# Kernel optimization log

Measured on AMD Instinct MI355X. Metric: run time of the kernel, lower is better.

## Reference

```python
import jax, jax.numpy as jnp
import numpy as np

B, N, C = 128, 1024, 1
N_TIMES = 2
NUM_SUBSTEPS = 279  # trunc(dt_Output/dt_sub)+1 for default params


def setup_inputs() -> dict:
    key = jax.random.key(0)
    # small amplitude: d_to_u multiplies spectrum by k (up to N/2), keep CFL stable
    x = jax.random.normal(key, (B, N, C), dtype=jnp.float32) * 1e-3
    return {
        "x": x,
        "nu_para": jnp.float32(-3.0),
        "dt_Output_para": jnp.float32(-3.0),
        "cRatio_para": jnp.float32(0.1),
        "nTimes": N_TIMES,
        "num_substeps": NUM_SUBSTEPS,
    }


def _forward(x, nu_para, dt_Output_para, cRatio_para, nTimes, num_substeps):
    n = x.shape[1]
    L = 2.0 * np.pi
    k = (2.0 * np.pi / L) * jnp.arange(n // 2 + 1, dtype=jnp.float32)  # [n//2+1]
    ik = 1j * k

    # reparameterized physical params (sigmoid squashing, as in the torch module)
    nu = jax.nn.sigmoid(nu_para) * (0.5 - 0.01) + 0.01
    dt_out = jax.nn.sigmoid(dt_Output_para) * (0.1 - 0.001) + 0.001
    cR = jax.nn.sigmoid(cRatio_para) * (2.0 - 0.5) + 0.5

    d = jnp.transpose(x, (0, 2, 1))  # [B, C, N]
    # d_to_u: u = irfft(1j * rfft(d) * k)
    u = jnp.fft.irfft(1j * jnp.fft.rfft(d) * k, n=n)

    dt = dt_out / num_substeps
    # q = 1 - dt*cR*(k + nu*(1j*k)^2) ; (1j*k)^2 = -k^2 so q is real-valued
    q = 1.0 - dt * cR * (k - nu * k * k)

    def substep(u, _):
        uhat = jnp.fft.rfft(u)
        u2hat = jnp.fft.rfft(0.5 * u * u)
        u_new = jnp.fft.irfft((uhat - dt * ik * u2hat) / q, n=n)
        return u_new, None

    def outer(u, _):
        u, _ = jax.lax.scan(substep, u, None, length=num_substeps)
        return u, u

    _, usol = jax.lax.scan(outer, u, None, length=nTimes)  # [T, B, C, N]
    T = usol.shape[0]
    # torch.cat(usol, dim=1): [B, T*C, N] with time-major ordering
    usol = jnp.moveaxis(usol, 0, 1).reshape(usol.shape[1], T * usol.shape[2], n)

    # u_to_d: d_hat = -1j*rfft(u); d_hat[...,1:] /= k[1:]; d_hat[...,0] = 0
    d_hat = -1j * jnp.fft.rfft(usol)
    safe_k = jnp.where(k > 0, k, 1.0)
    d_hat = jnp.where(k > 0, d_hat / safe_k, jnp.zeros((), dtype=d_hat.dtype))
    dsol = jnp.fft.irfft(d_hat, n=n)  # [B, T*C, N]

    return jnp.transpose(dsol, (0, 2, 1))  # [B, N, T*C]


def reference(x, nu_para, dt_Output_para, cRatio_para, nTimes, num_substeps):
    return _forward(x, nu_para, dt_Output_para, cRatio_para, nTimes, num_substeps)
```

## Files before the change

### kernel.cpp

```cpp
#include <hip/hip_runtime.h>
#include <math.h>

#define NFFT 1024
#define BLK  512

template <int CTRL>
__device__ __forceinline__ float dppf(float v) {
    return __int_as_float(__builtin_amdgcn_update_dpp(
        0, __float_as_int(v), CTRL, 0xF, 0xF, true));
}
__device__ __forceinline__ float qx1(float v) { return dppf<0xB1>(v); }
__device__ __forceinline__ float qx2(float v) { return dppf<0x4E>(v); }
__device__ __forceinline__ float xr4(float v) { return dppf<0x1B>(dppf<0x141>(v)); }
__device__ __forceinline__ float xr8(float v) { return dppf<0x128>(v); }

__device__ __forceinline__ void pswap16(float v, float& lo, float& hi) {
    auto r = __builtin_amdgcn_permlane16_swap(__float_as_int(v), __float_as_int(v),
                                              false, false);
    lo = __int_as_float(r[0]);
    hi = __int_as_float(r[1]);
}
__device__ __forceinline__ void pswap32(float v, float& lo, float& hi) {
    auto r = __builtin_amdgcn_permlane32_swap(__float_as_int(v), __float_as_int(v),
                                              false, false);
    lo = __int_as_float(r[0]);
    hi = __int_as_float(r[1]);
}

__global__ __launch_bounds__(BLK, 2)
void siva_kernel(const float* __restrict__ x,
                 const float* __restrict__ nu_p,
                 const float* __restrict__ dto_p,
                 const float* __restrict__ cr_p,
                 const int* __restrict__ nt_p,
                 const int* __restrict__ ns_p,
                 float* __restrict__ out) {
    __shared__ float4 bufF[BLK];
    __shared__ float4 bufI[BLK];

    const int tt = threadIdx.x;
    const int b  = blockIdx.x;
    const int l  = tt & 63;
    const int w  = tt >> 6;
    const int R  = (int)(__brev((unsigned)l) >> 26);

    const int nT   = nt_p[0];
    const int nsub = ns_p[0];

    const float nu  = (1.0f / (1.0f + expf(-nu_p[0])))  * (0.5f - 0.01f)  + 0.01f;
    const float dto = (1.0f / (1.0f + expf(-dto_p[0]))) * (0.1f - 0.001f) + 0.001f;
    const float cR  = (1.0f / (1.0f + expf(-cr_p[0])))  * (2.0f - 0.5f)   + 0.5f;
    const float dt   = dto / (float)nsub;
    const float dtcR = dt * cR;

    float2 T10;
    { const float a = (float)tt * (1.0f / 512.0f);
      T10 = make_float2(cospif(a), -sinpif(a)); }

    float2 E8f[8], D8[8];
    #pragma unroll
    for (int j = 0; j < 8; ++j) {
        const float af = (float)(j * w) * 0.25f + (float)(l * w) * (1.0f / 256.0f);
        E8f[j] = make_float2(cospif(af), -sinpif(af));
        const float ai = (float)(w * j) * 0.25f + (float)(l * j) * (1.0f / 256.0f);
        D8[j] = make_float2(cospif(ai), sinpif(ai));
    }

    float2 wf[6]; float sg[6]; float2 wi[6];
    #pragma unroll
    for (int s = 0; s < 6; ++s) {
        const int h = 32 >> s;
        const int lm = l & (h - 1);
        const bool hif = (l & h) != 0;
        const float a = (float)(lm * (32 / h)) * (1.0f / 32.0f);
        wf[s] = hif ? make_float2(cospif(a), -sinpif(a)) : make_float2(1.0f, 0.0f);
        sg[s] = hif ? -1.0f : 1.0f;
        const int h2 = 1 << s;
        const int lm2 = l & (h2 - 1);
        const float a2 = (float)lm2 / (float)h2;
        float2 wb = make_float2(cospif(a2), sinpif(a2));
        if ((l & h2) != 0) { wb.x = -wb.x; wb.y = -wb.y; }
        wi[s] = wb;
    }
    const bool m2 = (l & 2) != 0, m4 = (l & 4) != 0, m8 = (l & 8) != 0;

    float Sc[2], csn[2], si[2];
    #pragma unroll
    for (int p = 0; p < 2; ++p) {
        const int k = 16 * R + 2 * w + p;
        const float kk = (k <= 512) ? (float)k : (float)(k - 1024);
        const float ka = fabsf(kk);
        const float q  = 1.0f - dtcR * (ka - nu * ka * ka);
        const float a  = (1.0f / q) * (1.0f / 1024.0f);
        const float kkS = (k == 0 || k == 512) ? 0.0f : kk;
        Sc[p]  = a * (1.0f - dt * kkS);
        csn[p] = (k == 0) ? 0.0f : (1.0f / (1024.0f * kk));
        si[p]  = kk * (1.0f / 1024.0f);
    }
    float A2[2], B2[2];
    { const float sg1 = (l & 1) ? -1.0f : 1.0f;
      #pragma unroll
      for (int p = 0; p < 2; ++p) {
          const float so = __shfl_xor(Sc[p], 1);
          A2[p] = Sc[p] + so;
          B2[p] = sg1 * (Sc[p] - so);
      } }

    auto fwd_s = [&](float2& zz, float bx, float by, int s) {
        const float tx = fmaf(sg[s], zz.x, bx);
        const float ty = fmaf(sg[s], zz.y, by);
        zz.x = tx * wf[s].x - ty * wf[s].y;
        zz.y = tx * wf[s].y + ty * wf[s].x;
    };
    auto inv_s = [&](float2& zz, float bx, float by, int s, bool hi) {
        const float px = hi ? zz.x : bx, py = hi ? zz.y : by;
        const float qx = hi ? bx : zz.x, qy = hi ? by : zz.y;
        zz.x = qx + px * wi[s].x - py * wi[s].y;
        zz.y = qy + px * wi[s].y + py * wi[s].x;
    };

    auto lane_fwd5 = [&](float2 z[2]) {
        #pragma unroll
        for (int r = 0; r < 2; ++r) {
            float lox, hix, loy, hiy;
            pswap32(z[r].x, lox, hix); pswap32(z[r].y, loy, hiy);
            const float tx = fmaf(sg[0], hix, lox);
            const float ty = fmaf(sg[0], hiy, loy);
            z[r].x = tx * wf[0].x - ty * wf[0].y;
            z[r].y = tx * wf[0].y + ty * wf[0].x;
        }
        #pragma unroll
        for (int r = 0; r < 2; ++r) {
            float lox, hix, loy, hiy;
            pswap16(z[r].x, lox, hix); pswap16(z[r].y, loy, hiy);
            const float tx = fmaf(sg[1], hix, lox);
            const float ty = fmaf(sg[1], hiy, loy);
            z[r].x = tx * wf[1].x - ty * wf[1].y;
            z[r].y = tx * wf[1].y + ty * wf[1].x;
        }
        #pragma unroll
        for (int r = 0; r < 2; ++r) fwd_s(z[r], xr8(z[r].x), xr8(z[r].y), 2);
        #pragma unroll
        for (int r = 0; r < 2; ++r) fwd_s(z[r], xr4(z[r].x), xr4(z[r].y), 3);
        #pragma unroll
        for (int r = 0; r < 2; ++r) fwd_s(z[r], qx2(z[r].x), qx2(z[r].y), 4);
    };
    auto lane_inv5 = [&](float2 z[2]) {
        #pragma unroll
        for (int r = 0; r < 2; ++r) inv_s(z[r], qx2(z[r].x), qx2(z[r].y), 1, m2);
        #pragma unroll
        for (int r = 0; r < 2; ++r) inv_s(z[r], xr4(z[r].x), xr4(z[r].y), 2, m4);
        #pragma unroll
        for (int r = 0; r < 2; ++r) inv_s(z[r], xr8(z[r].x), xr8(z[r].y), 3, m8);
        #pragma unroll
        for (int r = 0; r < 2; ++r) {
            float lox, hix, loy, hiy;
            pswap16(z[r].x, lox, hix); pswap16(z[r].y, loy, hiy);
            z[r].x = fmaf(wi[4].x, hix, fmaf(-wi[4].y, hiy, lox));
            z[r].y = fmaf(wi[4].x, hiy, fmaf( wi[4].y, hix, loy));
        }
        #pragma unroll
        for (int r = 0; r < 2; ++r) {
            float lox, hix, loy, hiy;
            pswap32(z[r].x, lox, hix); pswap32(z[r].y, loy, hiy);
            z[r].x = fmaf(wi[5].x, hix, fmaf(-wi[5].y, hiy, lox));
            z[r].y = fmaf(wi[5].x, hiy, fmaf( wi[5].y, hix, loy));
        }
    };

    auto fwd_head = [&](float2 z[2]) {
        const float2 A  = make_float2(z[0].x + z[1].x, z[0].y + z[1].y);
        const float2 Dm = make_float2(z[0].x - z[1].x, z[0].y - z[1].y);
        const float2 Bc = make_float2(Dm.x * T10.x - Dm.y * T10.y,
                                      Dm.x * T10.y + Dm.y * T10.x);
        bufF[tt] = make_float4(A.x, A.y, Bc.x, Bc.y);
        __syncthreads();
        float2 za = make_float2(0.0f, 0.0f), zb = make_float2(0.0f, 0.0f);
        #pragma unroll
        for (int j = 0; j < 8; ++j) {
            const float4 v = bufF[64 * j + l];
            za.x = fmaf(E8f[j].x, v.x, za.x);  za.x = fmaf(-E8f[j].y, v.y, za.x);
            za.y = fmaf(E8f[j].x, v.y, za.y);  za.y = fmaf(E8f[j].y, v.x, za.y);
            zb.x = fmaf(E8f[j].x, v.z, zb.x);  zb.x = fmaf(-E8f[j].y, v.w, zb.x);
            zb.y = fmaf(E8f[j].x, v.w, zb.y);  zb.y = fmaf(E8f[j].y, v.z, zb.y);
        }
        z[0] = za; z[1] = zb;
        lane_fwd5(z);
    };

    auto inv_tail = [&](float2 z[2], float& u0o, float& u1o) {
        lane_inv5(z);
        bufI[tt] = make_float4(z[0].x, z[0].y, z[1].x, z[1].y);
        __syncthreads();
        float vAx = 0.0f, vBx = 0.0f, vBy = 0.0f;
        #pragma unroll
        for (int j = 0; j < 8; ++j) {
            const float4 v = bufI[64 * j + l];
            vAx = fmaf(D8[j].x, v.x, vAx);  vAx = fmaf(-D8[j].y, v.y, vAx);
            vBx = fmaf(D8[j].x, v.z, vBx);  vBx = fmaf(-D8[j].y, v.w, vBx);
            vBy = fmaf(D8[j].x, v.w, vBy);  vBy = fmaf(D8[j].y, v.z, vBy);
        }
        const float re = vBx * T10.x + vBy * T10.y;
        u0o = vAx + re;
        u1o = vAx - re;
    };

    float2 z[2];
    float u0, u1;
    z[0] = make_float2(x[b * NFFT + tt], 0.0f);
    z[1] = make_float2(x[b * NFFT + tt + 512], 0.0f);
    fwd_head(z);
    #pragma unroll
    for (int r = 0; r < 2; ++r) fwd_s(z[r], qx1(z[r].x), qx1(z[r].y), 5);
    #pragma unroll
    for (int p = 0; p < 2; ++p) {
        const float zx = z[p].x, zy = z[p].y;
        z[p] = make_float2(-zy * si[p], zx * si[p]);
    }
    { const bool m1 = (l & 1) != 0;
      #pragma unroll
      for (int r = 0; r < 2; ++r) inv_s(z[r], qx1(z[r].x), qx1(z[r].y), 0, m1); }
    inv_tail(z, u0, u1);

    for (int ot = 0; ot < nT; ++ot) {
        for (int ss = 0; ss < nsub; ++ss) {
            z[0] = make_float2(u0, 0.5f * u0 * u0);
            z[1] = make_float2(u1, 0.5f * u1 * u1);
            fwd_head(z);
            #pragma unroll
            for (int p = 0; p < 2; ++p) {
                const float px = qx1(z[p].x), py = qx1(z[p].y);
                z[p].x = fmaf(A2[p], z[p].x, B2[p] * px);
                z[p].y = fmaf(A2[p], z[p].y, B2[p] * py);
            }
            inv_tail(z, u0, u1);
        }
        z[0] = make_float2(u0, 0.0f);
        z[1] = make_float2(u1, 0.0f);
        fwd_head(z);
        #pragma unroll
        for (int r = 0; r < 2; ++r) fwd_s(z[r], qx1(z[r].x), qx1(z[r].y), 5);
        #pragma unroll
        for (int p = 0; p < 2; ++p) {
            const float zx = z[p].x, zy = z[p].y;
            z[p] = make_float2(zy * csn[p], -zx * csn[p]);
        }
        { const bool m1 = (l & 1) != 0;
          #pragma unroll
          for (int r = 0; r < 2; ++r) inv_s(z[r], qx1(z[r].x), qx1(z[r].y), 0, m1); }
        float d0, d1;
        inv_tail(z, d0, d1);
        out[(b * NFFT + tt) * nT + ot]       = d0;
        out[(b * NFFT + tt + 512) * nT + ot] = d1;
    }
}

extern "C" void kernel_launch(void* const* d_in, const int* in_sizes, int n_in,
                              void* d_out, int out_size, void* d_ws, size_t ws_size,
                              hipStream_t stream) {
    const float* x     = (const float*)d_in[0];
    const float* nu_p  = (const float*)d_in[1];
    const float* dto_p = (const float*)d_in[2];
    const float* cr_p  = (const float*)d_in[3];
    const int*   nt_p  = (const int*)d_in[4];
    const int*   ns_p  = (const int*)d_in[5];
    float* out = (float*)d_out;

    const int B = in_sizes[0] / NFFT;
    siva_kernel<<<B, BLK, 0, stream>>>(x, nu_p, dto_p, cr_p, nt_p, ns_p, out);
}
```

Baseline: 701.9 us.

## Fold last two FFT stages and spectral multiply into precomputed 4-lane matrix

Replaces the per-substep forward radix-2 stage 4, the diagonal spectral update, and inverse stages 0-1 with a single precomputed complex 4x4 quad-lane mixing matrix applied via DPP swizzles. It also rewrites the 8-point DFT in the forward head as a radix-2 factorized butterfly instead of a direct 8-term sum, and merges the per-stage twiddle select in inverse stages 2-3 into precomputed coefficient pairs. This cuts DPP and FMA work on the serial per-substep path. In exchange it adds register pressure from the precomputed matrices and a different floating-point rounding order.

New measurement: 707.3 us. Within noise of the previous version (+0.8%).

```diff
diff --git a/kernel.cpp b/kernel.cpp
--- a/kernel.cpp
+++ b/kernel.cpp
@@ -11,6 +11,7 @@
 }
 __device__ __forceinline__ float qx1(float v) { return dppf<0xB1>(v); }
 __device__ __forceinline__ float qx2(float v) { return dppf<0x4E>(v); }
+__device__ __forceinline__ float qx3(float v) { return dppf<0x1B>(v); }
 __device__ __forceinline__ float xr4(float v) { return dppf<0x1B>(dppf<0x141>(v)); }
 __device__ __forceinline__ float xr8(float v) { return dppf<0x128>(v); }
 
@@ -57,11 +58,18 @@
     { const float a = (float)tt * (1.0f / 512.0f);
       T10 = make_float2(cospif(a), -sinpif(a)); }
 
-    float2 E8f[8], D8[8];
+    const float pm = (w & 1) ? -1.0f : 1.0f;
+    float2 c4w, w8w, rotf;
+    { const float aw = 0.5f * (float)w;
+      c4w = make_float2(cospif(aw), -sinpif(aw));
+      const float aw8 = 0.25f * (float)w;
+      w8w = make_float2(cospif(aw8), -sinpif(aw8));
+      const float ar = (float)(l * w) * (1.0f / 256.0f);
+      rotf = make_float2(cospif(ar), -sinpif(ar)); }
+
+    float2 D8[8];
     #pragma unroll
     for (int j = 0; j < 8; ++j) {
-        const float af = (float)(j * w) * 0.25f + (float)(l * w) * (1.0f / 256.0f);
-        E8f[j] = make_float2(cospif(af), -sinpif(af));
         const float ai = (float)(w * j) * 0.25f + (float)(l * j) * (1.0f / 256.0f);
         D8[j] = make_float2(cospif(ai), sinpif(ai));
     }
@@ -82,7 +90,16 @@
         if ((l & h2) != 0) { wb.x = -wb.x; wb.y = -wb.y; }
         wi[s] = wb;
     }
-    const bool m2 = (l & 2) != 0, m4 = (l & 4) != 0, m8 = (l & 8) != 0;
+    const bool m1 = (l & 1) != 0, m2 = (l & 2) != 0,
+               m4 = (l & 4) != 0, m8 = (l & 8) != 0;
+
+    float2 cai[2], cbi[2];
+    #pragma unroll
+    for (int s = 2; s <= 3; ++s) {
+        const bool hif = (l & (1 << s)) != 0;
+        cai[s - 2] = hif ? wi[s] : make_float2(1.0f, 0.0f);
+        cbi[s - 2] = hif ? make_float2(1.0f, 0.0f) : wi[s];
+    }
 
     float Sc[2], csn[2], si[2];
     #pragma unroll
@@ -97,14 +114,41 @@
         csn[p] = (k == 0) ? 0.0f : (1.0f / (1024.0f * kk));
         si[p]  = kk * (1.0f / 1024.0f);
     }
-    float A2[2], B2[2];
-    { const float sg1 = (l & 1) ? -1.0f : 1.0f;
-      #pragma unroll
-      for (int p = 0; p < 2; ++p) {
-          const float so = __shfl_xor(Sc[p], 1);
-          A2[p] = Sc[p] + so;
-          B2[p] = sg1 * (Sc[p] - so);
-      } }
+
+    float2 Cq[2][4];
+    {
+        auto compose = [&](float2* o, const float2* bb, const float2* aa) {
+            #pragma unroll
+            for (int e = 0; e < 4; ++e) {
+                float cx = 0.0f, cy = 0.0f;
+                #pragma unroll
+                for (int d = 0; d < 4; ++d) {
+                    const float ax = __shfl_xor(aa[d ^ e].x, d);
+                    const float ay = __shfl_xor(aa[d ^ e].y, d);
+                    cx = fmaf(bb[d].x, ax, fmaf(-bb[d].y, ay, cx));
+                    cy = fmaf(bb[d].x, ay, fmaf(bb[d].y, ax, cy));
+                }
+                o[e] = make_float2(cx, cy);
+            }
+        };
+        const float2 one = make_float2(1.0f, 0.0f);
+        const float2 zer = make_float2(0.0f, 0.0f);
+        float2 Arow[4] = { make_float2(wf[4].x * sg[4], wf[4].y * sg[4]), zer,
+                           wf[4], zer };
+        float2 Brow[4] = { make_float2(sg[5], 0.0f), one, zer, zer };
+        float2 Erow[4] = { m1 ? wi[0] : one, m1 ? one : wi[0], zer, zer };
+        float2 Frow[4] = { m2 ? wi[1] : one, zer, m2 ? one : wi[1], zer };
+        float2 M1[4], M2[4], M3[4];
+        compose(M1, Brow, Arow);
+        #pragma unroll
+        for (int p = 0; p < 2; ++p) {
+            #pragma unroll
+            for (int e = 0; e < 4; ++e)
+                M2[e] = make_float2(Sc[p] * M1[e].x, Sc[p] * M1[e].y);
+            compose(M3, Erow, M2);
+            compose(Cq[p], Frow, M3);
+        }
+    }
 
     auto fwd_s = [&](float2& zz, float bx, float by, int s) {
         const float tx = fmaf(sg[s], zz.x, bx);
@@ -119,7 +163,7 @@
         zz.y = qy + px * wi[s].y + py * wi[s].x;
     };
 
-    auto lane_fwd5 = [&](float2 z[2]) {
+    auto lane_fwd4 = [&](float2 z[2]) {
         #pragma unroll
         for (int r = 0; r < 2; ++r) {
             float lox, hix, loy, hiy;
@@ -142,16 +186,26 @@
         for (int r = 0; r < 2; ++r) fwd_s(z[r], xr8(z[r].x), xr8(z[r].y), 2);
         #pragma unroll
         for (int r = 0; r < 2; ++r) fwd_s(z[r], xr4(z[r].x), xr4(z[r].y), 3);
-        #pragma unroll
-        for (int r = 0; r < 2; ++r) fwd_s(z[r], qx2(z[r].x), qx2(z[r].y), 4);
-    };
-    auto lane_inv5 = [&](float2 z[2]) {
-        #pragma unroll
-        for (int r = 0; r < 2; ++r) inv_s(z[r], qx2(z[r].x), qx2(z[r].y), 1, m2);
-        #pragma unroll
-        for (int r = 0; r < 2; ++r) inv_s(z[r], xr4(z[r].x), xr4(z[r].y), 2, m4);
-        #pragma unroll
-        for (int r = 0; r < 2; ++r) inv_s(z[r], xr8(z[r].x), xr8(z[r].y), 3, m8);
+    };
+    auto lane_inv4 = [&](float2 z[2]) {
+        #pragma unroll
+        for (int r = 0; r < 2; ++r) {
+            const float px = xr4(z[r].x), py = xr4(z[r].y);
+            const float nx = fmaf(cai[0].x, z[r].x, fmaf(-cai[0].y, z[r].y,
+                             fmaf(cbi[0].x, px, -cbi[0].y * py)));
+            const float ny = fmaf(cai[0].x, z[r].y, fmaf(cai[0].y, z[r].x,
+                             fmaf(cbi[0].x, py, cbi[0].y * px)));
+            z[r] = make_float2(nx, ny);
+        }
+        #pragma unroll
+        for (int r = 0; r < 2; ++r) {
+            const float px = xr8(z[r].x), py = xr8(z[r].y);
+            const float nx = fmaf(cai[1].x, z[r].x, fmaf(-cai[1].y, z[r].y,
+                             fmaf(cbi[1].x, px, -cbi[1].y * py)));
+            const float ny = fmaf(cai[1].x, z[r].y, fmaf(cai[1].y, z[r].x,
+                             fmaf(cbi[1].x, py, cbi[1].y * px)));
+            z[r] = make_float2(nx, ny);
+        }
         #pragma unroll
         for (int r = 0; r < 2; ++r) {
             float lox, hix, loy, hiy;
@@ -165,6 +219,24 @@
             pswap32(z[r].x, lox, hix); pswap32(z[r].y, loy, hiy);
             z[r].x = fmaf(wi[5].x, hix, fmaf(-wi[5].y, hiy, lox));
             z[r].y = fmaf(wi[5].x, hiy, fmaf( wi[5].y, hix, loy));
+        }
+    };
+
+    auto stageQuadC = [&](float2 z[2]) {
+        #pragma unroll
+        for (int p = 0; p < 2; ++p) {
+            const float x1 = qx1(z[p].x), y1 = qx1(z[p].y);
+            const float x2 = qx2(z[p].x), y2 = qx2(z[p].y);
+            const float x3 = qx3(z[p].x), y3 = qx3(z[p].y);
+            float nx = Cq[p][0].x * z[p].x - Cq[p][0].y * z[p].y;
+            float ny = Cq[p][0].x * z[p].y + Cq[p][0].y * z[p].x;
+            nx = fmaf(Cq[p][1].x, x1, fmaf(-Cq[p][1].y, y1, nx));
+            ny = fmaf(Cq[p][1].x, y1, fmaf( Cq[p][1].y, x1, ny));
+            nx = fmaf(Cq[p][2].x, x2, fmaf(-Cq[p][2].y, y2, nx));
+            ny = fmaf(Cq[p][2].x, y2, fmaf( Cq[p][2].y, x2, ny));
+            nx = fmaf(Cq[p][3].x, x3, fmaf(-Cq[p][3].y, y3, nx));
+            ny = fmaf(Cq[p][3].x, y3, fmaf( Cq[p][3].y, x3, ny));
+            z[p] = make_float2(nx, ny);
         }
     };
 
@@ -175,26 +247,49 @@
                                       Dm.x * T10.y + Dm.y * T10.x);
         bufF[tt] = make_float4(A.x, A.y, Bc.x, Bc.y);
         __syncthreads();
-        float2 za = make_float2(0.0f, 0.0f), zb = make_float2(0.0f, 0.0f);
-        #pragma unroll
-        for (int j = 0; j < 8; ++j) {
-            const float4 v = bufF[64 * j + l];
-            za.x = fmaf(E8f[j].x, v.x, za.x);  za.x = fmaf(-E8f[j].y, v.y, za.x);
-            za.y = fmaf(E8f[j].x, v.y, za.y);  za.y = fmaf(E8f[j].y, v.x, za.y);
-            zb.x = fmaf(E8f[j].x, v.z, zb.x);  zb.x = fmaf(-E8f[j].y, v.w, zb.x);
-            zb.y = fmaf(E8f[j].x, v.w, zb.y);  zb.y = fmaf(E8f[j].y, v.z, zb.y);
-        }
-        z[0] = za; z[1] = zb;
-        lane_fwd5(z);
+        float4 v[8];
+        #pragma unroll
+        for (int j = 0; j < 8; ++j) v[j] = bufF[64 * j + l];
+        {
+            const float a0x = fmaf(pm, v[4].x, v[0].x), a0y = fmaf(pm, v[4].y, v[0].y);
+            const float a1x = fmaf(pm, v[6].x, v[2].x), a1y = fmaf(pm, v[6].y, v[2].y);
+            const float a2x = fmaf(pm, v[5].x, v[1].x), a2y = fmaf(pm, v[5].y, v[1].y);
+            const float a3x = fmaf(pm, v[7].x, v[3].x), a3y = fmaf(pm, v[7].y, v[3].y);
+            const float Ex = fmaf(c4w.x, a1x, fmaf(-c4w.y, a1y, a0x));
+            const float Ey = fmaf(c4w.x, a1y, fmaf( c4w.y, a1x, a0y));
+            const float Fx = fmaf(c4w.x, a3x, fmaf(-c4w.y, a3y, a2x));
+            const float Fy = fmaf(c4w.x, a3y, fmaf( c4w.y, a3x, a2y));
+            const float Sx = fmaf(w8w.x, Fx, fmaf(-w8w.y, Fy, Ex));
+            const float Sy = fmaf(w8w.x, Fy, fmaf( w8w.y, Fx, Ey));
+            z[0] = make_float2(Sx * rotf.x - Sy * rotf.y,
+                               Sx * rotf.y + Sy * rotf.x);
+        }
+        {
+            const float a0x = fmaf(pm, v[4].z, v[0].z), a0y = fmaf(pm, v[4].w, v[0].w);
+            const float a1x = fmaf(pm, v[6].z, v[2].z), a1y = fmaf(pm, v[6].w, v[2].w);
+            const float a2x = fmaf(pm, v[5].z, v[1].z), a2y = fmaf(pm, v[5].w, v[1].w);
+            const float a3x = fmaf(pm, v[7].z, v[3].z), a3y = fmaf(pm, v[7].w, v[3].w);
+            const float Ex = fmaf(c4w.x, a1x, fmaf(-c4w.y, a1y, a0x));
+            const float Ey = fmaf(c4w.x, a1y, fmaf( c4w.y, a1x, a0y));
+            const float Fx = fmaf(c4w.x, a3x, fmaf(-c4w.y, a3y, a2x));
+            const float Fy = fmaf(c4w.x, a3y, fmaf( c4w.y, a3x, a2y));
+            const float Sx = fmaf(w8w.x, Fx, fmaf(-w8w.y, Fy, Ex));
+            const float Sy = fmaf(w8w.x, Fy, fmaf( w8w.y, Fx, Ey));
+            z[1] = make_float2(Sx * rotf.x - Sy * rotf.y,
+                               Sx * rotf.y + Sy * rotf.x);
+        }
+        lane_fwd4(z);
     };
 
     auto inv_tail = [&](float2 z[2], float& u0o, float& u1o) {
-        lane_inv5(z);
+        lane_inv4(z);
         bufI[tt] = make_float4(z[0].x, z[0].y, z[1].x, z[1].y);
         __syncthreads();
-        float vAx = 0.0f, vBx = 0.0f, vBy = 0.0f;
-        #pragma unroll
-        for (int j = 0; j < 8; ++j) {
+        float vAx, vBx, vBy;
+        { const float4 v0 = bufI[l];
+          vAx = v0.x; vBx = v0.z; vBy = v0.w; }
+        #pragma unroll
+        for (int j = 1; j < 8; ++j) {
             const float4 v = bufI[64 * j + l];
             vAx = fmaf(D8[j].x, v.x, vAx);  vAx = fmaf(-D8[j].y, v.y, vAx);
             vBx = fmaf(D8[j].x, v.z, vBx);  vBx = fmaf(-D8[j].y, v.w, vBx);
@@ -211,15 +306,18 @@
     z[1] = make_float2(x[b * NFFT + tt + 512], 0.0f);
     fwd_head(z);
     #pragma unroll
+    for (int r = 0; r < 2; ++r) fwd_s(z[r], qx2(z[r].x), qx2(z[r].y), 4);
+    #pragma unroll
     for (int r = 0; r < 2; ++r) fwd_s(z[r], qx1(z[r].x), qx1(z[r].y), 5);
     #pragma unroll
     for (int p = 0; p < 2; ++p) {
         const float zx = z[p].x, zy = z[p].y;
         z[p] = make_float2(-zy * si[p], zx * si[p]);
     }
-    { const bool m1 = (l & 1) != 0;
-      #pragma unroll
-      for (int r = 0; r < 2; ++r) inv_s(z[r], qx1(z[r].x), qx1(z[r].y), 0, m1); }
+    #pragma unroll
+    for (int r = 0; r < 2; ++r) inv_s(z[r], qx1(z[r].x), qx1(z[r].y), 0, m1);
+    #pragma unroll
+    for (int r = 0; r < 2; ++r) inv_s(z[r], qx2(z[r].x), qx2(z[r].y), 1, m2);
     inv_tail(z, u0, u1);
 
     for (int ot = 0; ot < nT; ++ot) {
@@ -227,27 +325,25 @@
             z[0] = make_float2(u0, 0.5f * u0 * u0);
             z[1] = make_float2(u1, 0.5f * u1 * u1);
             fwd_head(z);
-            #pragma unroll
-            for (int p = 0; p < 2; ++p) {
-                const float px = qx1(z[p].x), py = qx1(z[p].y);
-                z[p].x = fmaf(A2[p], z[p].x, B2[p] * px);
-                z[p].y = fmaf(A2[p], z[p].y, B2[p] * py);
-            }
+            stageQuadC(z);
             inv_tail(z, u0, u1);
         }
         z[0] = make_float2(u0, 0.0f);
         z[1] = make_float2(u1, 0.0f);
         fwd_head(z);
         #pragma unroll
+        for (int r = 0; r < 2; ++r) fwd_s(z[r], qx2(z[r].x), qx2(z[r].y), 4);
+        #pragma unroll
         for (int r = 0; r < 2; ++r) fwd_s(z[r], qx1(z[r].x), qx1(z[r].y), 5);
         #pragma unroll
         for (int p = 0; p < 2; ++p) {
             const float zx = z[p].x, zy = z[p].y;
             z[p] = make_float2(zy * csn[p], -zx * csn[p]);
         }
-        { const bool m1 = (l & 1) != 0;
-          #pragma unroll
-          for (int r = 0; r < 2; ++r) inv_s(z[r], qx1(z[r].x), qx1(z[r].y), 0, m1); }
+        #pragma unroll
+        for (int r = 0; r < 2; ++r) inv_s(z[r], qx1(z[r].x), qx1(z[r].y), 0, m1);
+        #pragma unroll
+        for (int r = 0; r < 2; ++r) inv_s(z[r], qx2(z[r].x), qx2(z[r].y), 1, m2);
         float d0, d1;
         inv_tail(z, d0, d1);
         out[(b * NFFT + tt) * nT + ot]       = d0;
```

## Fuse spectral multiply into single LDS exchange via precomputed circulant rows

Applied to the files above, without the earlier changes.

Each substep now does a 64-point in-lane FFT, then one LDS exchange, then a 64-point inverse. Before, it did two exchanges with separate 8-point DFT stages plus a spectral multiply. The diagonal spectral operator and the 8-point outer stages are folded into per-thread 16x2 complex coefficient rows, built once with trig at setup. This halves the __syncthreads and LDS round trips per substep and drops the twiddle/T10 work. In exchange it adds more FMAs per exchange (a 16-point dense mix instead of 8), more registers for the 64 floats of coefficients, and costly one-time row construction that could hurt occupancy.

Result: slower. 2.652 ms (+277.9%).

```diff
diff --git a/kernel.cpp b/kernel.cpp
--- a/kernel.cpp
+++ b/kernel.cpp
@@ -35,14 +35,15 @@
                  const int* __restrict__ nt_p,
                  const int* __restrict__ ns_p,
                  float* __restrict__ out) {
-    __shared__ float4 bufF[BLK];
-    __shared__ float4 bufI[BLK];
+    __shared__ float4 buf[2][BLK];
 
     const int tt = threadIdx.x;
     const int b  = blockIdx.x;
     const int l  = tt & 63;
     const int w  = tt >> 6;
-    const int R  = (int)(__brev((unsigned)l) >> 26);
+    const int a0 = 2 * w;
+    const int a1 = 2 * w + 1;
+    const int kb = (int)(__brev((unsigned)l) >> 26);
 
     const int nT   = nt_p[0];
     const int nsub = ns_p[0];
@@ -52,19 +53,6 @@
     const float cR  = (1.0f / (1.0f + expf(-cr_p[0])))  * (2.0f - 0.5f)   + 0.5f;
     const float dt   = dto / (float)nsub;
     const float dtcR = dt * cR;
-
-    float2 T10;
-    { const float a = (float)tt * (1.0f / 512.0f);
-      T10 = make_float2(cospif(a), -sinpif(a)); }
-
-    float2 E8f[8], D8[8];
-    #pragma unroll
-    for (int j = 0; j < 8; ++j) {
-        const float af = (float)(j * w) * 0.25f + (float)(l * w) * (1.0f / 256.0f);
-        E8f[j] = make_float2(cospif(af), -sinpif(af));
-        const float ai = (float)(w * j) * 0.25f + (float)(l * j) * (1.0f / 256.0f);
-        D8[j] = make_float2(cospif(ai), sinpif(ai));
-    }
 
     float2 wf[6]; float sg[6]; float2 wi[6];
     #pragma unroll
@@ -82,29 +70,61 @@
         if ((l & h2) != 0) { wb.x = -wb.x; wb.y = -wb.y; }
         wi[s] = wb;
     }
-    const bool m2 = (l & 2) != 0, m4 = (l & 4) != 0, m8 = (l & 8) != 0;
-
-    float Sc[2], csn[2], si[2];
+    float2 cai[4], cbi[4];
     #pragma unroll
-    for (int p = 0; p < 2; ++p) {
-        const int k = 16 * R + 2 * w + p;
+    for (int s = 0; s < 4; ++s) {
+        const bool hif = (l & (1 << s)) != 0;
+        cai[s] = hif ? wi[s] : make_float2(1.0f, 0.0f);
+        cbi[s] = hif ? make_float2(1.0f, 0.0f) : wi[s];
+    }
+
+    float mS[16];
+    #pragma unroll
+    for (int ka = 0; ka < 16; ++ka) {
+        const int k = kb + 64 * ka;
         const float kk = (k <= 512) ? (float)k : (float)(k - 1024);
-        const float ka = fabsf(kk);
-        const float q  = 1.0f - dtcR * (ka - nu * ka * ka);
-        const float a  = (1.0f / q) * (1.0f / 1024.0f);
+        const float kab = fabsf(kk);
+        const float q = 1.0f - dtcR * (kab - nu * kab * kab);
         const float kkS = (k == 0 || k == 512) ? 0.0f : kk;
-        Sc[p]  = a * (1.0f - dt * kkS);
-        csn[p] = (k == 0) ? 0.0f : (1.0f / (1024.0f * kk));
-        si[p]  = kk * (1.0f / 1024.0f);
-    }
-    float A2[2], B2[2];
-    { const float sg1 = (l & 1) ? -1.0f : 1.0f;
-      #pragma unroll
-      for (int p = 0; p < 2; ++p) {
-          const float so = __shfl_xor(Sc[p], 1);
-          A2[p] = Sc[p] + so;
-          B2[p] = sg1 * (Sc[p] - so);
-      } }
+        mS[ka] = (1.0f - dt * kkS) / q;
+    }
+
+    auto buildRows = [&](const float* m, float2* r0, float2* r1) {
+        #pragma unroll
+        for (int aq = 0; aq < 16; ++aq) {
+            {
+                const float d = (float)(aq - a0);
+                float sx = 0.0f, sy = 0.0f;
+                #pragma unroll
+                for (int ka = 0; ka < 16; ++ka) {
+                    const float ang = d * (float)ka * 0.125f;
+                    sx = fmaf(m[ka], cospif(ang), sx);
+                    sy = fmaf(m[ka], -sinpif(ang), sy);
+                }
+                const float angb = d * (float)kb * (1.0f / 512.0f);
+                const float cb = cospif(angb), sb = -sinpif(angb);
+                r0[aq] = make_float2((cb * sx - sb * sy) * (1.0f / 1024.0f),
+                                     (cb * sy + sb * sx) * (1.0f / 1024.0f));
+            }
+            {
+                const float d = (float)(aq - a1);
+                float sx = 0.0f, sy = 0.0f;
+                #pragma unroll
+                for (int ka = 0; ka < 16; ++ka) {
+                    const float ang = d * (float)ka * 0.125f;
+                    sx = fmaf(m[ka], cospif(ang), sx);
+                    sy = fmaf(m[ka], -sinpif(ang), sy);
+                }
+                const float angb = d * (float)kb * (1.0f / 512.0f);
+                const float cb = cospif(angb), sb = -sinpif(angb);
+                r1[aq] = make_float2((cb * sx - sb * sy) * (1.0f / 1024.0f),
+                                     (cb * sy + sb * sx) * (1.0f / 1024.0f));
+            }
+        }
+    };
+
+    float2 rS0[16], rS1[16];
+    buildRows(mS, rS0, rS1);
 
     auto fwd_s = [&](float2& zz, float bx, float by, int s) {
         const float tx = fmaf(sg[s], zz.x, bx);
@@ -112,14 +132,15 @@
         zz.x = tx * wf[s].x - ty * wf[s].y;
         zz.y = tx * wf[s].y + ty * wf[s].x;
     };
-    auto inv_s = [&](float2& zz, float bx, float by, int s, bool hi) {
-        const float px = hi ? zz.x : bx, py = hi ? zz.y : by;
-        const float qx = hi ? bx : zz.x, qy = hi ? by : zz.y;
-        zz.x = qx + px * wi[s].x - py * wi[s].y;
-        zz.y = qy + px * wi[s].y + py * wi[s].x;
-    };
-
-    auto lane_fwd5 = [&](float2 z[2]) {
+    auto inv_sf = [&](float2& zz, float px, float py, int s) {
+        const float nx = fmaf(cai[s].x, zz.x, fmaf(-cai[s].y, zz.y,
+                         fmaf(cbi[s].x, px, -cbi[s].y * py)));
+        const float ny = fmaf(cai[s].x, zz.y, fmaf(cai[s].y, zz.x,
+                         fmaf(cbi[s].x, py, cbi[s].y * px)));
+        zz = make_float2(nx, ny);
+    };
+
+    auto lane_fwd6 = [&](float2 z[2]) {
         #pragma unroll
         for (int r = 0; r < 2; ++r) {
             float lox, hix, loy, hiy;
@@ -144,14 +165,18 @@
         for (int r = 0; r < 2; ++r) fwd_s(z[r], xr4(z[r].x), xr4(z[r].y), 3);
         #pragma unroll
         for (int r = 0; r < 2; ++r) fwd_s(z[r], qx2(z[r].x), qx2(z[r].y), 4);
-    };
-    auto lane_inv5 = [&](float2 z[2]) {
-        #pragma unroll
-        for (int r = 0; r < 2; ++r) inv_s(z[r], qx2(z[r].x), qx2(z[r].y), 1, m2);
-        #pragma unroll
-        for (int r = 0; r < 2; ++r) inv_s(z[r], xr4(z[r].x), xr4(z[r].y), 2, m4);
-        #pragma unroll
-        for (int r = 0; r < 2; ++r) inv_s(z[r], xr8(z[r].x), xr8(z[r].y), 3, m8);
+        #pragma unroll
+        for (int r = 0; r < 2; ++r) fwd_s(z[r], qx1(z[r].x), qx1(z[r].y), 5);
+    };
+    auto lane_inv6 = [&](float2 z[2]) {
+        #pragma unroll
+        for (int r = 0; r < 2; ++r) inv_sf(z[r], qx1(z[r].x), qx1(z[r].y), 0);
+        #pragma unroll
+        for (int r = 0; r < 2; ++r) inv_sf(z[r], qx2(z[r].x), qx2(z[r].y), 1);
+        #pragma unroll
+        for (int r = 0; r < 2; ++r) inv_sf(z[r], xr4(z[r].x), xr4(z[r].y), 2);
+        #pragma unroll
+        for (int r = 0; r < 2; ++r) inv_sf(z[r], xr8(z[r].x), xr8(z[r].y), 3);
         #pragma unroll
         for (int r = 0; r < 2; ++r) {
             float lox, hix, loy, hiy;
@@ -168,90 +193,78 @@
         }
     };
 
-    auto fwd_head = [&](float2 z[2]) {
-        const float2 A  = make_float2(z[0].x + z[1].x, z[0].y + z[1].y);
-        const float2 Dm = make_float2(z[0].x - z[1].x, z[0].y - z[1].y);
-        const float2 Bc = make_float2(Dm.x * T10.x - Dm.y * T10.y,
-                                      Dm.x * T10.y + Dm.y * T10.x);
-        bufF[tt] = make_float4(A.x, A.y, Bc.x, Bc.y);
+    int par = 0;
+    auto exchange = [&](float2 z[2], const float2* r0, const float2* r1) {
+        buf[par][tt] = make_float4(z[0].x, z[0].y, z[1].x, z[1].y);
         __syncthreads();
-        float2 za = make_float2(0.0f, 0.0f), zb = make_float2(0.0f, 0.0f);
-        #pragma unroll
-        for (int j = 0; j < 8; ++j) {
-            const float4 v = bufF[64 * j + l];
-            za.x = fmaf(E8f[j].x, v.x, za.x);  za.x = fmaf(-E8f[j].y, v.y, za.x);
-            za.y = fmaf(E8f[j].x, v.y, za.y);  za.y = fmaf(E8f[j].y, v.x, za.y);
-            zb.x = fmaf(E8f[j].x, v.z, zb.x);  zb.x = fmaf(-E8f[j].y, v.w, zb.x);
-            zb.y = fmaf(E8f[j].x, v.w, zb.y);  zb.y = fmaf(E8f[j].y, v.z, zb.y);
-        }
-        z[0] = za; z[1] = zb;
-        lane_fwd5(z);
-    };
-
-    auto inv_tail = [&](float2 z[2], float& u0o, float& u1o) {
-        lane_inv5(z);
-        bufI[tt] = make_float4(z[0].x, z[0].y, z[1].x, z[1].y);
-        __syncthreads();
-        float vAx = 0.0f, vBx = 0.0f, vBy = 0.0f;
-        #pragma unroll
-        for (int j = 0; j < 8; ++j) {
-            const float4 v = bufI[64 * j + l];
-            vAx = fmaf(D8[j].x, v.x, vAx);  vAx = fmaf(-D8[j].y, v.y, vAx);
-            vBx = fmaf(D8[j].x, v.z, vBx);  vBx = fmaf(-D8[j].y, v.w, vBx);
-            vBy = fmaf(D8[j].x, v.w, vBy);  vBy = fmaf(D8[j].y, v.z, vBy);
-        }
-        const float re = vBx * T10.x + vBy * T10.y;
-        u0o = vAx + re;
-        u1o = vAx - re;
+        float ax0 = 0.0f, ay0 = 0.0f, ax1 = 0.0f, ay1 = 0.0f;
+        #pragma unroll
+        for (int wq = 0; wq < 8; ++wq) {
+            const float4 v = buf[par][wq * 64 + l];
+            const float2 cA0 = r0[2 * wq], cB0 = r0[2 * wq + 1];
+            const float2 cA1 = r1[2 * wq], cB1 = r1[2 * wq + 1];
+            ax0 = fmaf(cA0.x, v.x, ax0);  ax0 = fmaf(-cA0.y, v.y, ax0);
+            ay0 = fmaf(cA0.x, v.y, ay0);  ay0 = fmaf( cA0.y, v.x, ay0);
+            ax0 = fmaf(cB0.x, v.z, ax0);  ax0 = fmaf(-cB0.y, v.w, ax0);
+            ay0 = fmaf(cB0.x, v.w, ay0);  ay0 = fmaf( cB0.y, v.z, ay0);
+            ax1 = fmaf(cA1.x, v.x, ax1);  ax1 = fmaf(-cA1.y, v.y, ax1);
+            ay1 = fmaf(cA1.x, v.y, ay1);  ay1 = fmaf( cA1.y, v.x, ay1);
+            ax1 = fmaf(cB1.x, v.z, ax1);  ax1 = fmaf(-cB1.y, v.w, ax1);
+            ay1 = fmaf(cB1.x, v.w, ay1);  ay1 = fmaf( cB1.y, v.z, ay1);
+        }
+        z[0] = make_float2(ax0, ay0);
+        z[1] = make_float2(ax1, ay1);
+        par ^= 1;
     };
 
     float2 z[2];
     float u0, u1;
-    z[0] = make_float2(x[b * NFFT + tt], 0.0f);
-    z[1] = make_float2(x[b * NFFT + tt + 512], 0.0f);
-    fwd_head(z);
-    #pragma unroll
-    for (int r = 0; r < 2; ++r) fwd_s(z[r], qx1(z[r].x), qx1(z[r].y), 5);
-    #pragma unroll
-    for (int p = 0; p < 2; ++p) {
-        const float zx = z[p].x, zy = z[p].y;
-        z[p] = make_float2(-zy * si[p], zx * si[p]);
-    }
-    { const bool m1 = (l & 1) != 0;
-      #pragma unroll
-      for (int r = 0; r < 2; ++r) inv_s(z[r], qx1(z[r].x), qx1(z[r].y), 0, m1); }
-    inv_tail(z, u0, u1);
+    z[0] = make_float2(x[b * NFFT + 16 * l + a0], 0.0f);
+    z[1] = make_float2(x[b * NFFT + 16 * l + a1], 0.0f);
+    {
+        float mD[16];
+        #pragma unroll
+        for (int ka = 0; ka < 16; ++ka) {
+            const int k = kb + 64 * ka;
+            mD[ka] = (k <= 512) ? (float)k : (float)(k - 1024);
+        }
+        float2 rD0[16], rD1[16];
+        buildRows(mD, rD0, rD1);
+        lane_fwd6(z);
+        exchange(z, rD0, rD1);
+        lane_inv6(z);
+        u0 = -z[0].y;
+        u1 = -z[1].y;
+    }
 
     for (int ot = 0; ot < nT; ++ot) {
         for (int ss = 0; ss < nsub; ++ss) {
             z[0] = make_float2(u0, 0.5f * u0 * u0);
             z[1] = make_float2(u1, 0.5f * u1 * u1);
-            fwd_head(z);
+            lane_fwd6(z);
+            exchange(z, rS0, rS1);
+            lane_inv6(z);
+            u0 = z[0].x;
+            u1 = z[1].x;
+        }
+        {
+            float mU[16];
             #pragma unroll
-            for (int p = 0; p < 2; ++p) {
-                const float px = qx1(z[p].x), py = qx1(z[p].y);
-                z[p].x = fmaf(A2[p], z[p].x, B2[p] * px);
-                z[p].y = fmaf(A2[p], z[p].y, B2[p] * py);
+            for (int ka = 0; ka < 16; ++ka) {
+                const int k = kb + 64 * ka;
+                const float kk = (k <= 512) ? (float)k : (float)(k - 1024);
+                mU[ka] = (k == 0) ? 0.0f : (1.0f / kk);
             }
-            inv_tail(z, u0, u1);
-        }
-        z[0] = make_float2(u0, 0.0f);
-        z[1] = make_float2(u1, 0.0f);
-        fwd_head(z);
-        #pragma unroll
-        for (int r = 0; r < 2; ++r) fwd_s(z[r], qx1(z[r].x), qx1(z[r].y), 5);
-        #pragma unroll
-        for (int p = 0; p < 2; ++p) {
-            const float zx = z[p].x, zy = z[p].y;
-            z[p] = make_float2(zy * csn[p], -zx * csn[p]);
-        }
-        { const bool m1 = (l & 1) != 0;
-          #pragma unroll
-          for (int r = 0; r < 2; ++r) inv_s(z[r], qx1(z[r].x), qx1(z[r].y), 0, m1); }
-        float d0, d1;
-        inv_tail(z, d0, d1);
-        out[(b * NFFT + tt) * nT + ot]       = d0;
-        out[(b * NFFT + tt + 512) * nT + ot] = d1;
+            float2 rU0[16], rU1[16];
+            buildRows(mU, rU0, rU1);
+            z[0] = make_float2(u0, 0.0f);
+            z[1] = make_float2(u1, 0.0f);
+            lane_fwd6(z);
+            exchange(z, rU0, rU1);
+            lane_inv6(z);
+            out[(b * NFFT + 16 * l + a0) * nT + ot] = z[0].y;
+            out[(b * NFFT + 16 * l + a1) * nT + ot] = z[1].y;
+        }
     }
 }
 
```
